# Optimization experiments

Hardware: AMD Instinct MI355X
Metric: run time of the kernel (lower is better)

## Reference

```python
import jax, jax.numpy as jnp
import numpy as np
import math

N_HEADS = 16
STRIDE = 4
LN_EPS = 1e-5
ROPE_BASE = 10000.0


def rotate_half(x):
    h = x.shape[-1] // 2
    return jnp.concatenate([-x[..., h:], x[..., :h]], axis=-1)


def rope_cos_sin(seq_len, head_dim, dtype):
    inv_freq = 1.0 / (ROPE_BASE ** (jnp.arange(0, head_dim, 2, dtype=jnp.float32) / head_dim))
    t = jnp.arange(seq_len, dtype=jnp.float32)
    freqs = jnp.outer(t, inv_freq)                      # [S, hd/2]
    emb = jnp.concatenate([freqs, freqs], axis=-1)      # [S, hd]
    return jnp.cos(emb).astype(dtype), jnp.sin(emb).astype(dtype)


def linear_upsample(x, T):
    # x: [B, Ts, D] -> [B, T, D]; matches F.interpolate(mode='linear', align_corners=False)
    Ts = x.shape[1]
    scale = Ts / T
    src = (jnp.arange(T, dtype=jnp.float32) + 0.5) * scale - 0.5
    src = jnp.clip(src, 0.0, Ts - 1.0)
    i0 = jnp.floor(src).astype(jnp.int32)
    i1 = jnp.minimum(i0 + 1, Ts - 1)
    w = (src - i0.astype(jnp.float32)).astype(x.dtype)[None, :, None]
    return x[:, i0, :] * (1.0 - w) + x[:, i1, :] * w


def setup_inputs() -> dict:
    key = jax.random.key(0)
    ks = jax.random.split(key, 4)
    B, T, D = 4, 4096, 1024
    s = 1.0 / math.sqrt(D)
    return {
        "x": jax.random.normal(ks[0], (B, T, D), dtype=jnp.float32),
        "norm_w": jnp.ones((D,), dtype=jnp.float32),
        "norm_b": jnp.zeros((D,), dtype=jnp.float32),
        "W_qkv": jax.random.normal(ks[1], (D, 3 * D), dtype=jnp.float32) * s,
        "b_qkv": jnp.zeros((3 * D,), dtype=jnp.float32),
        "W_out": jax.random.normal(ks[2], (D, D), dtype=jnp.float32) * s,
        "b_out": jnp.zeros((D,), dtype=jnp.float32),
    }


def reference(x, norm_w, norm_b, W_qkv, b_qkv, W_out, b_out):
    B, T, D = x.shape
    H = N_HEADS
    hd = D // H
    residual = x

    # LayerNorm (biased variance, eps=1e-5)
    mu = jnp.mean(x, axis=-1, keepdims=True)
    var = jnp.var(x, axis=-1, keepdims=True)
    x_norm = (x - mu) * jax.lax.rsqrt(var + LN_EPS) * norm_w + norm_b

    # strided downsample (T >= 2*stride path)
    xs = x_norm[:, ::STRIDE, :]
    Ts = xs.shape[1]

    # fused QKV projection
    qkv = xs @ W_qkv + b_qkv                             # [B, Ts, 3D]
    qkv = qkv.reshape(B, Ts, 3, H, hd).transpose(2, 0, 3, 1, 4)
    q, k, v = qkv[0], qkv[1], qkv[2]                     # [B, H, Ts, hd]

    # RoPE
    cos, sin = rope_cos_sin(Ts, hd, q.dtype)             # [Ts, hd]
    q = q * cos + rotate_half(q) * sin
    k = k * cos + rotate_half(k) * sin

    # causal SDPA on strided subsequence
    scores = jnp.einsum('bhqd,bhkd->bhqk', q, k) / math.sqrt(hd)
    causal = jnp.tril(jnp.ones((Ts, Ts), dtype=bool))
    scores = jnp.where(causal, scores, jnp.finfo(scores.dtype).min)
    attn = jax.nn.softmax(scores, axis=-1)
    out = jnp.einsum('bhqk,bhkd->bhqd', attn, v)         # [B, H, Ts, hd]
    out = out.transpose(0, 2, 1, 3).reshape(B, Ts, D)

    out = out @ W_out + b_out
    out = linear_upsample(out, T)                        # [B, T, D]
    return residual + out
```

## Files before the change

### kernel.cpp

```cpp
#include <hip/hip_runtime.h>
#include <hip/hip_bf16.h>

#define DEVFN __device__ __forceinline__

typedef float f32x4 __attribute__((ext_vector_type(4)));
typedef float f32x16 __attribute__((ext_vector_type(16)));
typedef __bf16 bf16x8 __attribute__((ext_vector_type(8)));
typedef unsigned short u16x8 __attribute__((ext_vector_type(8)));
typedef unsigned short u16x4 __attribute__((ext_vector_type(4)));
typedef unsigned u32x4 __attribute__((ext_vector_type(4)));

DEVFN unsigned short f2bf(float f) {
  unsigned u = __builtin_bit_cast(unsigned, f);
  u = (u + 0x7FFFu + ((u >> 16) & 1u)) >> 16;
  return (unsigned short)u;
}

DEVFN float bf2f(unsigned short s) {
  return __builtin_bit_cast(float, (unsigned)s << 16);
}

DEVFN f32x4 mfma_bf16(u16x8 a, u16x8 b, f32x4 c) {
  return __builtin_amdgcn_mfma_f32_16x16x32_bf16((bf16x8)a, (bf16x8)b, c, 0, 0, 0);
}

DEVFN f32x16 mfma32(u16x8 a, u16x8 b, f32x16 c) {
  return __builtin_amdgcn_mfma_f32_32x32x16_bf16((bf16x8)a, (bf16x8)b, c, 0, 0, 0);
}

DEVFN unsigned cvt_pk_bf16(float a, float b) {
  unsigned r;
  asm("v_cvt_pk_bf16_f32 %0, %1, %2" : "=v"(r) : "v"(a), "v"(b));
  return r;
}

DEVFN void permswap(unsigned& a, unsigned& b) {
  asm("v_permlane32_swap_b32 %0, %1" : "+v"(a), "+v"(b));
}

DEVFN void sincos_rev(float rev, float* sn, float* cs) {
  float fr, s, c;
  asm("v_fract_f32 %0, %1" : "=v"(fr) : "v"(rev));
  asm("v_sin_f32 %0, %1" : "=v"(s) : "v"(fr));
  asm("v_cos_f32 %0, %1" : "=v"(c) : "v"(fr));
  *sn = s; *cs = c;
}

DEVFN void gload_lds16(const void* g, void* l) {
  __builtin_amdgcn_global_load_lds(
      (const __attribute__((address_space(1))) void*)g,
      (__attribute__((address_space(3))) void*)l, 16, 0, 0);
}

__global__ __launch_bounds__(256) void prologue_kernel(
    const float* __restrict__ x, const float* __restrict__ w,
    const float* __restrict__ bb, unsigned short* __restrict__ xs,
    const float* __restrict__ Wq, unsigned short* __restrict__ Wtq,
    const float* __restrict__ Wo, unsigned short* __restrict__ Wto,
    int T, int Ts, int D, int stride, int M) {
  __shared__ float tile[32][33];
  __shared__ float ps[4], pq[4];
  int bid = blockIdx.x;
  int t = threadIdx.x;
  if (bid < M) {
    int b = bid / Ts, ts = bid - b * Ts;
    const float* xr = x + ((size_t)b * T + (size_t)ts * stride) * D;
    float4 v = *(const float4*)(xr + t * 4);
    float s = v.x + v.y + v.z + v.w;
    float sq = v.x * v.x + v.y * v.y + v.z * v.z + v.w * v.w;
#pragma unroll
    for (int m = 1; m < 64; m <<= 1) { s += __shfl_xor(s, m); sq += __shfl_xor(sq, m); }
    if ((t & 63) == 0) { ps[t >> 6] = s; pq[t >> 6] = sq; }
    __syncthreads();
    s = ps[0] + ps[1] + ps[2] + ps[3];
    sq = pq[0] + pq[1] + pq[2] + pq[3];
    float invD = 1.0f / (float)D;
    float mu = s * invD;
    float var = sq * invD - mu * mu;
    float rs = rsqrtf(var + 1e-5f);
    int c = t * 4;
    float4 wv = *(const float4*)(w + c);
    float4 bv = *(const float4*)(bb + c);
    u16x4 o;
    o[0] = f2bf((v.x - mu) * rs * wv.x + bv.x);
    o[1] = f2bf((v.y - mu) * rs * wv.y + bv.y);
    o[2] = f2bf((v.z - mu) * rs * wv.z + bv.z);
    o[3] = f2bf((v.w - mu) * rs * wv.w + bv.w);
    *(u16x4*)(xs + (size_t)bid * D + c) = o;
  } else {
    const float* W; unsigned short* Wt; int N, b2;
    b2 = bid - M;
    if (b2 < (3 * D / 32) * (D / 32)) { W = Wq; Wt = Wtq; N = 3 * D; }
    else { b2 -= (3 * D / 32) * (D / 32); W = Wo; Wt = Wto; N = D; }
    int nb = N / 32;
    int n0 = (b2 % nb) * 32, k0 = (b2 / nb) * 32;
    int tx = t & 31, ty = t >> 5;
#pragma unroll
    for (int i = 0; i < 32; i += 8) tile[ty + i][tx] = W[(size_t)(k0 + ty + i) * N + n0 + tx];
    __syncthreads();
#pragma unroll
    for (int i = 0; i < 32; i += 8) Wt[(size_t)(n0 + ty + i) * D + k0 + tx] = f2bf(tile[tx][ty + i]);
  }
}

__global__ __launch_bounds__(512, 1) void gemm_qkv256_kernel(
    const unsigned short* __restrict__ A, const unsigned short* __restrict__ Bt,
    const float* __restrict__ bias, int M, int N, int Kd,
    unsigned short* __restrict__ Qo, unsigned short* __restrict__ Ko,
    unsigned short* __restrict__ Vt) {
  __shared__ __align__(128) char lds[131072];
  const int tid = threadIdx.x, l = tid & 63, w = tid >> 6;
  const int wr = w >> 2, wc = w & 3;
  const int lg = l >> 4, lr = l & 15;
  const int o = blockIdx.x;
  const int xcd = o & 7, s = o >> 3;
  const int bm = (xcd & 3) * 4 + (s & 3);
  const int bn = (xcd >> 2) * 6 + (s >> 2);
  const int m0 = bm << 8, n0 = bn << 8;
  const int chk = (lg ^ ((lr >> 1) & 3)) << 4;

  f32x4 acc[8][4] = {};

#define STAGE32(kk, bufoff)                                                 \
  do {                                                                      \
    _Pragma("unroll")                                                       \
    for (int i_ = 0; i_ < 2; i_++) {                                        \
      int c_ = tid + (i_ << 9);                                             \
      int rl_ = c_ >> 2, c4_ = c_ & 3;                                      \
      int cs_ = c4_ ^ ((rl_ >> 1) & 3);                                     \
      gload_lds16(A + (size_t)(m0 + rl_) * Kd + (kk) + cs_ * 8,             \
                  lds + (bufoff) + c_ * 16);                                \
      gload_lds16(Bt + (size_t)(n0 + rl_) * Kd + (kk) + cs_ * 8,            \
                  lds + (bufoff) + 16384 + c_ * 16);                        \
    }                                                                       \
  } while (0)

  STAGE32(0, 0);
  STAGE32(32, 32768);
  STAGE32(64, 65536);

  const int NT = Kd >> 5;
  for (int t = 0; t < NT; ++t) {
    if (t < NT - 2)       asm volatile("s_waitcnt vmcnt(8)" ::: "memory");
    else if (t == NT - 2) asm volatile("s_waitcnt vmcnt(4)" ::: "memory");
    else                  asm volatile("s_waitcnt vmcnt(0)" ::: "memory");
    __builtin_amdgcn_s_barrier();
    const int curoff = (t & 3) << 15;

    u16x8 bfr[4], afr[8];
#pragma unroll
    for (int nf = 0; nf < 4; nf++)
      bfr[nf] = *(const u16x8*)(lds + curoff + 16384 +
                                (wc * 64 + nf * 16 + lr) * 64 + chk);
#pragma unroll
    for (int mf = 0; mf < 8; mf++)
      afr[mf] = *(const u16x8*)(lds + curoff +
                                (wr * 128 + mf * 16 + lr) * 64 + chk);
    if (t + 3 < NT) STAGE32((t + 3) << 5, ((t + 3) & 3) << 15);
    asm volatile("s_waitcnt lgkmcnt(0)" ::: "memory");
    __builtin_amdgcn_sched_barrier(0);
    __builtin_amdgcn_s_setprio(1);
#pragma unroll
    for (int mf = 0; mf < 8; mf++)
#pragma unroll
      for (int nf = 0; nf < 4; nf++)
        acc[mf][nf] = mfma_bf16(afr[mf], bfr[nf], acc[mf][nf]);
    __builtin_amdgcn_s_setprio(0);
    __builtin_amdgcn_s_barrier();
  }
#undef STAGE32

  int nb = n0 + wc * 64;
  int which = nb >> 10;
  int h = (nb & 1023) >> 6;
  if (which < 2) {
    unsigned short* dst = (which == 0) ? Qo : Ko;
    float qsc = (which == 0) ? 0.18033688f : 1.0f;
#pragma unroll
    for (int nt = 0; nt < 2; nt++) {
      int d = nt * 16 + lr;
      float invf_rev = exp2f((float)d * -0.41524101f) * 0.15915494f;
      float blo = bias[nb + nt * 16 + lr];
      float bhi = bias[nb + (nt + 2) * 16 + lr];
#pragma unroll
      for (int mt = 0; mt < 8; mt++) {
        int mb = m0 + wr * 128 + mt * 16 + lg * 4;
#pragma unroll
        for (int r = 0; r < 4; r++) {
          int m = mb + r;
          int b_ = m >> 10, ts = m & 1023;
          float va = acc[mt][nt][r] + blo;
          float vb = acc[mt][nt + 2][r] + bhi;
          float sn, cs;
          sincos_rev((float)ts * invf_rev, &sn, &cs);
          size_t base = (((size_t)(b_ * 16 + h)) * 1024 + ts) * 64;
          dst[base + d] = f2bf((va * cs - vb * sn) * qsc);
          dst[base + d + 32] = f2bf((vb * cs + va * sn) * qsc);
        }
      }
    }
  } else {
#pragma unroll
    for (int nt = 0; nt < 4; nt++) {
      int d = nt * 16 + lr;
      float bi = bias[nb + nt * 16 + lr];
#pragma unroll
      for (int mt = 0; mt < 8; mt++) {
        int mb = m0 + wr * 128 + mt * 16 + lg * 4;
        int b_ = mb >> 10, tsb = mb & 1023;
        u16x4 pk;
#pragma unroll
        for (int r = 0; r < 4; r++) pk[r] = f2bf(acc[mt][nt][r] + bi);
        *(u16x4*)(Vt + (size_t)(b_ * 16 + h) * 65536 +
                  (size_t)(tsb >> 5) * 2048 + d * 32 + (tsb & 31)) = pk;
      }
    }
  }
}

__global__ __launch_bounds__(256) void gemm_out_kernel(
    const unsigned short* __restrict__ A, const unsigned short* __restrict__ Bt,
    const float* __restrict__ bias, int M, int N, int Kd,
    unsigned short* __restrict__ Co) {
  __shared__ __align__(128) char lds[49152];
  const int tid = threadIdx.x, l = tid & 63, w = tid >> 6;
  const int wr = w >> 1, wc = w & 1;
  const int lg = l >> 4, lr = l & 15;
  const int o = blockIdx.x;
  const int xcd = o & 7, s = o >> 3;
  const int bm = xcd * 4 + (s & 3);
  const int bn = s >> 2;
  const int m0 = bm << 7, n0 = bn << 7;
  const int chk = (lg ^ ((lr >> 1) & 3)) << 4;

#define STAGE32O(kk, bufoff)                                                \
  do {                                                                      \
    _Pragma("unroll")                                                       \
    for (int i_ = 0; i_ < 2; i_++) {                                        \
      int c_ = tid + (i_ << 8);                                             \
      int rl_ = c_ >> 2, c4_ = c_ & 3;                                      \
      int cs_ = c4_ ^ ((rl_ >> 1) & 3);                                     \
      gload_lds16(A + (size_t)(m0 + rl_) * Kd + (kk) + cs_ * 8,             \
                  lds + (bufoff) + c_ * 16);                                \
      gload_lds16(Bt + (size_t)(n0 + rl_) * Kd + (kk) + cs_ * 8,            \
                  lds + (bufoff) + 8192 + c_ * 16);                         \
    }                                                                       \
  } while (0)

  f32x4 acc[4][4] = {};
  STAGE32O(0, 0);
  STAGE32O(32, 16384);

  const int NT = Kd >> 5;
  for (int t = 0; t < NT; ++t) {
    if (t < NT - 1) asm volatile("s_waitcnt vmcnt(4)" ::: "memory");
    else            asm volatile("s_waitcnt vmcnt(0)" ::: "memory");
    __builtin_amdgcn_s_barrier();
    const int curoff = (t % 3) * 16384;

    u16x8 bfr[4], afr[4];
#pragma unroll
    for (int nf = 0; nf < 4; nf++)
      bfr[nf] = *(const u16x8*)(lds + curoff + 8192 +
                                (wc * 64 + nf * 16 + lr) * 64 + chk);
#pragma unroll
    for (int mf = 0; mf < 4; mf++)
      afr[mf] = *(const u16x8*)(lds + curoff +
                                (wr * 64 + mf * 16 + lr) * 64 + chk);
    if (t + 2 < NT) STAGE32O((t + 2) << 5, ((t + 2) % 3) * 16384);
    asm volatile("s_waitcnt lgkmcnt(0)" ::: "memory");
    __builtin_amdgcn_sched_barrier(0);
    __builtin_amdgcn_s_setprio(1);
#pragma unroll
    for (int mf = 0; mf < 4; mf++)
#pragma unroll
      for (int nf = 0; nf < 4; nf++)
        acc[mf][nf] = mfma_bf16(afr[mf], bfr[nf], acc[mf][nf]);
    __builtin_amdgcn_s_setprio(0);
    __builtin_amdgcn_s_barrier();
  }
#undef STAGE32O

#pragma unroll
  for (int nt = 0; nt < 4; nt++) {
    int n = n0 + wc * 64 + nt * 16 + lr;
    float bi = bias[n];
#pragma unroll
    for (int mt = 0; mt < 4; mt++) {
      int mb = m0 + wr * 64 + mt * 16 + lg * 4;
#pragma unroll
      for (int r = 0; r < 4; r++)
        Co[(size_t)(mb + r) * N + n] = f2bf(acc[mt][nt][r] + bi);
    }
  }
}

__global__ __launch_bounds__(256) void attn_kernel(
    const unsigned short* __restrict__ Q, const unsigned short* __restrict__ K,
    const unsigned short* __restrict__ Vt, unsigned short* __restrict__ O,
    int Ts, int H) {
  __shared__ __align__(128) char kvlds[2][16384];
  int t = threadIdx.x, w = t >> 6, l = t & 63;
  int h2 = l >> 5, lq = l & 31;
  int bh = blockIdx.x & 63;
  int i = blockIdx.x >> 6;
  int qg = (i < 4) ? 7 - i : i - 4;
  int b = bh / H, hh = bh % H;
  int qw0 = qg * 128 + w * 32;

  const unsigned short* Qh = Q + ((size_t)bh * Ts) * 64;
  const unsigned short* Kh = K + ((size_t)bh * Ts) * 64;
  const unsigned short* Vh = Vt + (size_t)bh * 65536;

  u16x8 qf[4];
#pragma unroll
  for (int c = 0; c < 4; c++)
    qf[c] = *(const u16x8*)(Qh + (size_t)(qw0 + lq) * 64 + c * 16 + h2 * 8);

#define STAGE_KV(jt, buf)                                                   \
  do {                                                                      \
    _Pragma("unroll")                                                       \
    for (int i_ = 0; i_ < 2; i_++) {                                        \
      int c_ = t + (i_ << 8);                                               \
      int r_ = c_ >> 3, jg_ = c_ & 7;                                       \
      gload_lds16(Kh + (size_t)(jt) * 4096 + r_ * 64 + ((jg_ ^ (r_ & 7)) << 3), \
                  kvlds[buf] + c_ * 16);                                    \
    }                                                                       \
    {                                                                       \
      int d_ = t >> 2, g_ = t & 3;                                          \
      int gs_ = (g_ ^ ((d_ >> 1) & 3)) << 3;                                \
      gload_lds16(Vh + (size_t)(2 * (jt)) * 2048 + d_ * 32 + gs_,           \
                  kvlds[buf] + 8192 + t * 16);                              \
      gload_lds16(Vh + (size_t)(2 * (jt) + 1) * 2048 + d_ * 32 + gs_,       \
                  kvlds[buf] + 12288 + t * 16);                             \
    }                                                                       \
  } while (0)

  f32x16 olo = {}, ohi = {};
  float mrow = -1e30f, lsum = 0.f;
  const int sk = lq & 7;
  const int sv = (lq >> 1) & 3;

  int ntiles = 2 * qg + 2;
  STAGE_KV(0, 0);

  for (int jt = 0; jt < ntiles; jt++) {
    __syncthreads();
    int cur = jt & 1;
    if (jt + 1 < ntiles) STAGE_KV(jt + 1, cur ^ 1);

    int kvt = jt * 64;
    if (kvt > qw0) continue;
    bool haveS1 = (kvt + 32 <= qw0);
    bool diag0 = (kvt == qw0);
    bool diag1 = (kvt + 32 == qw0);

    const char* kb0 = kvlds[cur] + lq * 128;
    const char* kb1 = kvlds[cur] + (32 + lq) * 128;
    u16x8 kf0[4], kf1[4];
#pragma unroll
    for (int c = 0; c < 4; c++)
      kf0[c] = *(const u16x8*)(kb0 + (((c << 1) + h2) ^ sk) * 16);
    f32x16 sA = {}, sB = {};
    if (haveS1) {
#pragma unroll
      for (int c = 0; c < 4; c++)
        kf1[c] = *(const u16x8*)(kb1 + (((c << 1) + h2) ^ sk) * 16);
      __builtin_amdgcn_s_setprio(1);
#pragma unroll
      for (int c = 0; c < 4; c++) sA = mfma32(kf0[c], qf[c], sA);
#pragma unroll
      for (int c = 0; c < 4; c++) sB = mfma32(kf1[c], qf[c], sB);
      __builtin_amdgcn_s_setprio(0);
    } else {
      __builtin_amdgcn_s_setprio(1);
#pragma unroll
      for (int c = 0; c < 4; c++) sA = mfma32(kf0[c], qf[c], sA);
      __builtin_amdgcn_s_setprio(0);
    }

    float p[32];
#pragma unroll
    for (int r = 0; r < 16; r++) {
      float v = sA[r];
      if (diag0) {
        int kvl = (r & 3) + 8 * (r >> 2) + 4 * h2;
        v = (kvl > lq) ? -1e30f : v;
      }
      p[r] = v;
    }
#pragma unroll
    for (int r = 0; r < 16; r++) {
      float v = haveS1 ? sB[r] : -1e30f;
      if (diag1) {
        int kvl = (r & 3) + 8 * (r >> 2) + 4 * h2;
        v = (kvl > lq) ? -1e30f : v;
      }
      p[16 + r] = v;
    }

    float m16[16], m8[8], m4[4];
#pragma unroll
    for (int r = 0; r < 16; r++) m16[r] = fmaxf(p[r], p[16 + r]);
#pragma unroll
    for (int r = 0; r < 8; r++) m8[r] = fmaxf(m16[r], m16[r + 8]);
#pragma unroll
    for (int r = 0; r < 4; r++) m4[r] = fmaxf(m8[r], m8[r + 4]);
    float tmax = fmaxf(fmaxf(m4[0], m4[2]), fmaxf(m4[1], m4[3]));
    tmax = fmaxf(tmax, __shfl_xor(tmax, 32));

    if (!__all(tmax <= mrow + 8.0f)) {
      float mnew = fmaxf(mrow, tmax);
      float al = exp2f(mrow - mnew);
      mrow = mnew;
      lsum *= al;
      olo *= al;
      ohi *= al;
    }

#pragma unroll
    for (int r = 0; r < 32; r++) p[r] = exp2f(p[r] - mrow);
    float s16[16], s8[8], s4[4];
#pragma unroll
    for (int r = 0; r < 16; r++) s16[r] = p[r] + p[16 + r];
#pragma unroll
    for (int r = 0; r < 8; r++) s8[r] = s16[r] + s16[r + 8];
#pragma unroll
    for (int r = 0; r < 4; r++) s4[r] = s8[r] + s8[r + 4];
    lsum += (s4[0] + s4[2]) + (s4[1] + s4[3]);

    {
      unsigned a01 = cvt_pk_bf16(p[0], p[1]),   a23 = cvt_pk_bf16(p[2], p[3]);
      unsigned a45 = cvt_pk_bf16(p[4], p[5]),   a67 = cvt_pk_bf16(p[6], p[7]);
      unsigned a89 = cvt_pk_bf16(p[8], p[9]),   aAB = cvt_pk_bf16(p[10], p[11]);
      unsigned aCD = cvt_pk_bf16(p[12], p[13]), aEF = cvt_pk_bf16(p[14], p[15]);
      permswap(a01, a45);
      permswap(a23, a67);
      permswap(a89, aCD);
      permswap(aAB, aEF);
      u32x4 f0 = {a01, a23, a45, a67};
      u32x4 f1 = {a89, aAB, aCD, aEF};
      u16x8 P0 = __builtin_bit_cast(u16x8, f0);
      u16x8 P1 = __builtin_bit_cast(u16x8, f1);

      const char* vb_ = kvlds[cur] + 8192;
      u16x8 vf[4];
      vf[0] = *(const u16x8*)(vb_ + lq * 64 + ((0 + h2) ^ sv) * 16);
      vf[1] = *(const u16x8*)(vb_ + lq * 64 + ((2 + h2) ^ sv) * 16);
      vf[2] = *(const u16x8*)(vb_ + (32 + lq) * 64 + ((0 + h2) ^ sv) * 16);
      vf[3] = *(const u16x8*)(vb_ + (32 + lq) * 64 + ((2 + h2) ^ sv) * 16);
      __builtin_amdgcn_s_setprio(1);
      olo = mfma32(vf[0], P0, olo);
      olo = mfma32(vf[1], P1, olo);
      ohi = mfma32(vf[2], P0, ohi);
      ohi = mfma32(vf[3], P1, ohi);
      __builtin_amdgcn_s_setprio(0);
    }

    if (haveS1) {
      unsigned b01 = cvt_pk_bf16(p[16], p[17]), b23 = cvt_pk_bf16(p[18], p[19]);
      unsigned b45 = cvt_pk_bf16(p[20], p[21]), b67 = cvt_pk_bf16(p[22], p[23]);
      unsigned b89 = cvt_pk_bf16(p[24], p[25]), bAB = cvt_pk_bf16(p[26], p[27]);
      unsigned bCD = cvt_pk_bf16(p[28], p[29]), bEF = cvt_pk_bf16(p[30], p[31]);
      permswap(b01, b45);
      permswap(b23, b67);
      permswap(b89, bCD);
      permswap(bAB, bEF);
      u32x4 g0 = {b01, b23, b45, b67};
      u32x4 g1 = {b89, bAB, bCD, bEF};
      u16x8 Q0 = __builtin_bit_cast(u16x8, g0);
      u16x8 Q1 = __builtin_bit_cast(u16x8, g1);

      const char* vb_ = kvlds[cur] + 8192 + 4096;
      u16x8 vf[4];
      vf[0] = *(const u16x8*)(vb_ + lq * 64 + ((0 + h2) ^ sv) * 16);
      vf[1] = *(const u16x8*)(vb_ + lq * 64 + ((2 + h2) ^ sv) * 16);
      vf[2] = *(const u16x8*)(vb_ + (32 + lq) * 64 + ((0 + h2) ^ sv) * 16);
      vf[3] = *(const u16x8*)(vb_ + (32 + lq) * 64 + ((2 + h2) ^ sv) * 16);
      __builtin_amdgcn_s_setprio(1);
      olo = mfma32(vf[0], Q0, olo);
      olo = mfma32(vf[1], Q1, olo);
      ohi = mfma32(vf[2], Q0, ohi);
      ohi = mfma32(vf[3], Q1, ohi);
      __builtin_amdgcn_s_setprio(0);
    }
  }
#undef STAGE_KV

  lsum += __shfl_xor(lsum, 32);
  float inv = 1.0f / lsum;
  int q = qw0 + lq;
  unsigned short* orow = O + ((size_t)b * Ts + q) * (size_t)(H * 64) + hh * 64;
#pragma unroll
  for (int g = 0; g < 4; g++) {
    u16x4 plo, phi;
#pragma unroll
    for (int j2 = 0; j2 < 4; j2++) {
      plo[j2] = f2bf(olo[g * 4 + j2] * inv);
      phi[j2] = f2bf(ohi[g * 4 + j2] * inv);
    }
    *(u16x4*)(orow + g * 8 + h2 * 4) = plo;
    *(u16x4*)(orow + 32 + g * 8 + h2 * 4) = phi;
  }
}

__global__ __launch_bounds__(256) void upsample_kernel(
    const float* __restrict__ x, const unsigned short* __restrict__ proj,
    float* __restrict__ out, int T, int Ts, int D) {
  int bk = blockIdx.x;
  int b = bk / Ts, k = bk - b * Ts;
  int d4 = threadIdx.x;
  size_t prow = (size_t)b * Ts * D;
  u16x4 av = *((const u16x4*)(proj + prow + (size_t)max(k - 1, 0) * D) + d4);
  u16x4 bv = *((const u16x4*)(proj + prow + (size_t)k * D) + d4);
  u16x4 cv = *((const u16x4*)(proj + prow + (size_t)min(k + 1, Ts - 1) * D) + d4);
  f32x4 a, bb, c;
#pragma unroll
  for (int j = 0; j < 4; j++) {
    a[j] = bf2f(av[j]); bb[j] = bf2f(bv[j]); c[j] = bf2f(cv[j]);
  }

  size_t xbase = ((size_t)b * T + 4 * (size_t)k) * D + (size_t)d4 * 4;
  f32x4 x0 = __builtin_nontemporal_load((const f32x4*)(x + xbase));
  f32x4 x1 = __builtin_nontemporal_load((const f32x4*)(x + xbase + D));
  f32x4 x2 = __builtin_nontemporal_load((const f32x4*)(x + xbase + 2 * D));
  f32x4 x3 = __builtin_nontemporal_load((const f32x4*)(x + xbase + 3 * D));

  f32x4 o0 = x0 + 0.375f * a + 0.625f * bb;
  f32x4 o1 = x1 + 0.125f * a + 0.875f * bb;
  f32x4 o2 = x2 + 0.875f * bb + 0.125f * c;
  f32x4 o3 = x3 + 0.625f * bb + 0.375f * c;

  __builtin_nontemporal_store(o0, (f32x4*)(out + xbase));
  __builtin_nontemporal_store(o1, (f32x4*)(out + xbase + D));
  __builtin_nontemporal_store(o2, (f32x4*)(out + xbase + 2 * D));
  __builtin_nontemporal_store(o3, (f32x4*)(out + xbase + 3 * D));
}

extern "C" void kernel_launch(void* const* d_in, const int* in_sizes, int n_in,
                              void* d_out, int out_size, void* d_ws, size_t ws_size,
                              hipStream_t stream) {
  (void)in_sizes; (void)n_in; (void)out_size; (void)ws_size;
  const float* x = (const float*)d_in[0];
  const float* norm_w = (const float*)d_in[1];
  const float* norm_b = (const float*)d_in[2];
  const float* W_qkv = (const float*)d_in[3];
  const float* b_qkv = (const float*)d_in[4];
  const float* W_out = (const float*)d_in[5];
  const float* b_out = (const float*)d_in[6];
  float* out = (float*)d_out;

  const int B = 4, T = 4096, D = 1024, H = 16, STR = 4;
  const int Ts = T / STR;
  const int M = B * Ts;

  char* ws = (char*)d_ws;
  unsigned short* xs  = (unsigned short*)(ws);
  unsigned short* Wtq = (unsigned short*)(ws + ((size_t)8 << 20));
  unsigned short* Wto = (unsigned short*)(ws + ((size_t)14 << 20));
  unsigned short* Qb  = (unsigned short*)(ws + ((size_t)16 << 20));
  unsigned short* Kb  = (unsigned short*)(ws + ((size_t)24 << 20));
  unsigned short* Vtb = (unsigned short*)(ws + ((size_t)32 << 20));
  unsigned short* proj = (unsigned short*)(ws + ((size_t)16 << 20));
  unsigned short* att = xs;

  prologue_kernel<<<M + (3 * D / 32) * (D / 32) + (D / 32) * (D / 32), 256, 0, stream>>>(
      x, norm_w, norm_b, xs, W_qkv, Wtq, W_out, Wto, T, Ts, D, STR, M);
  gemm_qkv256_kernel<<<(M / 256) * (3 * D / 256), 512, 0, stream>>>(
      xs, Wtq, b_qkv, M, 3 * D, D, Qb, Kb, Vtb);
  attn_kernel<<<B * H * 8, 256, 0, stream>>>(Qb, Kb, Vtb, att, Ts, H);
  gemm_out_kernel<<<(M / 128) * (D / 128), 256, 0, stream>>>(
      att, Wto, b_out, M, D, D, proj);
  upsample_kernel<<<B * Ts, 256, 0, stream>>>(x, proj, out, T, Ts, D);
}
```

Measured before the change: 118.4 us.

## Split attention KV loop across warps per 32-query tile with LDS merge

The attention kernel now gives each block a single 32-query tile and splits its causal KV tiles across the four warps in strided fashion. K and V fragments are read straight from global memory instead of being staged through double-buffered LDS. The per-warp partial softmax states are then merged through shared memory in a two-step reduction. This launches more blocks and balances causal work better, at the cost of uncoalesced global K/V reads, no K/V reuse across warps, and extra merge synchronisation.

```diff
diff --git a/kernel.cpp b/kernel.cpp
--- a/kernel.cpp
+++ b/kernel.cpp
@@ -299,14 +299,12 @@
     const unsigned short* __restrict__ Q, const unsigned short* __restrict__ K,
     const unsigned short* __restrict__ Vt, unsigned short* __restrict__ O,
     int Ts, int H) {
-  __shared__ __align__(128) char kvlds[2][16384];
   int t = threadIdx.x, w = t >> 6, l = t & 63;
   int h2 = l >> 5, lq = l & 31;
   int bh = blockIdx.x & 63;
-  int i = blockIdx.x >> 6;
-  int qg = (i < 4) ? 7 - i : i - 4;
+  int qt = 31 - (blockIdx.x >> 6);
   int b = bh / H, hh = bh % H;
-  int qw0 = qg * 128 + w * 32;
+  int q0 = qt * 32;
 
   const unsigned short* Qh = Q + ((size_t)bh * Ts) * 64;
   const unsigned short* Kh = K + ((size_t)bh * Ts) * 64;
@@ -315,95 +313,46 @@
   u16x8 qf[4];
 #pragma unroll
   for (int c = 0; c < 4; c++)
-    qf[c] = *(const u16x8*)(Qh + (size_t)(qw0 + lq) * 64 + c * 16 + h2 * 8);
-
-#define STAGE_KV(jt, buf)                                                   \
-  do {                                                                      \
-    _Pragma("unroll")                                                       \
-    for (int i_ = 0; i_ < 2; i_++) {                                        \
-      int c_ = t + (i_ << 8);                                               \
-      int r_ = c_ >> 3, jg_ = c_ & 7;                                       \
-      gload_lds16(Kh + (size_t)(jt) * 4096 + r_ * 64 + ((jg_ ^ (r_ & 7)) << 3), \
-                  kvlds[buf] + c_ * 16);                                    \
-    }                                                                       \
-    {                                                                       \
-      int d_ = t >> 2, g_ = t & 3;                                          \
-      int gs_ = (g_ ^ ((d_ >> 1) & 3)) << 3;                                \
-      gload_lds16(Vh + (size_t)(2 * (jt)) * 2048 + d_ * 32 + gs_,           \
-                  kvlds[buf] + 8192 + t * 16);                              \
-      gload_lds16(Vh + (size_t)(2 * (jt) + 1) * 2048 + d_ * 32 + gs_,       \
-                  kvlds[buf] + 12288 + t * 16);                             \
-    }                                                                       \
-  } while (0)
+    qf[c] = *(const u16x8*)(Qh + (size_t)(q0 + lq) * 64 + c * 16 + h2 * 8);
+
+  const unsigned short* kb = Kh + (size_t)lq * 64 + h2 * 8;
+  const unsigned short* vb = Vh + (size_t)lq * 32 + h2 * 8;
 
   f32x16 olo = {}, ohi = {};
   float mrow = -1e30f, lsum = 0.f;
-  const int sk = lq & 7;
-  const int sv = (lq >> 1) & 3;
-
-  int ntiles = 2 * qg + 2;
-  STAGE_KV(0, 0);
-
-  for (int jt = 0; jt < ntiles; jt++) {
-    __syncthreads();
-    int cur = jt & 1;
-    if (jt + 1 < ntiles) STAGE_KV(jt + 1, cur ^ 1);
-
-    int kvt = jt * 64;
-    if (kvt > qw0) continue;
-    bool haveS1 = (kvt + 32 <= qw0);
-    bool diag0 = (kvt == qw0);
-    bool diag1 = (kvt + 32 == qw0);
-
-    const char* kb0 = kvlds[cur] + lq * 128;
-    const char* kb1 = kvlds[cur] + (32 + lq) * 128;
-    u16x8 kf0[4], kf1[4];
-#pragma unroll
-    for (int c = 0; c < 4; c++)
-      kf0[c] = *(const u16x8*)(kb0 + (((c << 1) + h2) ^ sk) * 16);
-    f32x16 sA = {}, sB = {};
-    if (haveS1) {
-#pragma unroll
-      for (int c = 0; c < 4; c++)
-        kf1[c] = *(const u16x8*)(kb1 + (((c << 1) + h2) ^ sk) * 16);
-      __builtin_amdgcn_s_setprio(1);
-#pragma unroll
-      for (int c = 0; c < 4; c++) sA = mfma32(kf0[c], qf[c], sA);
-#pragma unroll
-      for (int c = 0; c < 4; c++) sB = mfma32(kf1[c], qf[c], sB);
-      __builtin_amdgcn_s_setprio(0);
-    } else {
-      __builtin_amdgcn_s_setprio(1);
-#pragma unroll
-      for (int c = 0; c < 4; c++) sA = mfma32(kf0[c], qf[c], sA);
-      __builtin_amdgcn_s_setprio(0);
-    }
-
-    float p[32];
+
+  for (int j = w; j <= qt; j += 4) {
+    const unsigned short* kt = kb + (size_t)j * 2048;
+    const unsigned short* vt = vb + (size_t)j * 2048;
+    u16x8 kf[4], vf[4];
+#pragma unroll
+    for (int c = 0; c < 4; c++) kf[c] = *(const u16x8*)(kt + c * 16);
+    vf[0] = *(const u16x8*)(vt);
+    vf[1] = *(const u16x8*)(vt + 16);
+    vf[2] = *(const u16x8*)(vt + 1024);
+    vf[3] = *(const u16x8*)(vt + 1024 + 16);
+
+    f32x16 s = {};
+    __builtin_amdgcn_s_setprio(1);
+#pragma unroll
+    for (int c = 0; c < 4; c++) s = mfma32(kf[c], qf[c], s);
+    __builtin_amdgcn_s_setprio(0);
+
+    bool diag = (j == qt);
+    float p[16];
 #pragma unroll
     for (int r = 0; r < 16; r++) {
-      float v = sA[r];
-      if (diag0) {
+      float v = s[r];
+      if (diag) {
         int kvl = (r & 3) + 8 * (r >> 2) + 4 * h2;
         v = (kvl > lq) ? -1e30f : v;
       }
       p[r] = v;
     }
-#pragma unroll
-    for (int r = 0; r < 16; r++) {
-      float v = haveS1 ? sB[r] : -1e30f;
-      if (diag1) {
-        int kvl = (r & 3) + 8 * (r >> 2) + 4 * h2;
-        v = (kvl > lq) ? -1e30f : v;
-      }
-      p[16 + r] = v;
-    }
-
-    float m16[16], m8[8], m4[4];
-#pragma unroll
-    for (int r = 0; r < 16; r++) m16[r] = fmaxf(p[r], p[16 + r]);
-#pragma unroll
-    for (int r = 0; r < 8; r++) m8[r] = fmaxf(m16[r], m16[r + 8]);
+
+    float m8[8], m4[4];
+#pragma unroll
+    for (int r = 0; r < 8; r++) m8[r] = fmaxf(p[r], p[r + 8]);
 #pragma unroll
     for (int r = 0; r < 4; r++) m4[r] = fmaxf(m8[r], m8[r + 4]);
     float tmax = fmaxf(fmaxf(m4[0], m4[2]), fmaxf(m4[1], m4[3]));
@@ -419,88 +368,90 @@
     }
 
 #pragma unroll
-    for (int r = 0; r < 32; r++) p[r] = exp2f(p[r] - mrow);
-    float s16[16], s8[8], s4[4];
-#pragma unroll
-    for (int r = 0; r < 16; r++) s16[r] = p[r] + p[16 + r];
-#pragma unroll
-    for (int r = 0; r < 8; r++) s8[r] = s16[r] + s16[r + 8];
+    for (int r = 0; r < 16; r++) p[r] = exp2f(p[r] - mrow);
+    float s8[8], s4[4];
+#pragma unroll
+    for (int r = 0; r < 8; r++) s8[r] = p[r] + p[r + 8];
 #pragma unroll
     for (int r = 0; r < 4; r++) s4[r] = s8[r] + s8[r + 4];
     lsum += (s4[0] + s4[2]) + (s4[1] + s4[3]);
 
-    {
-      unsigned a01 = cvt_pk_bf16(p[0], p[1]),   a23 = cvt_pk_bf16(p[2], p[3]);
-      unsigned a45 = cvt_pk_bf16(p[4], p[5]),   a67 = cvt_pk_bf16(p[6], p[7]);
-      unsigned a89 = cvt_pk_bf16(p[8], p[9]),   aAB = cvt_pk_bf16(p[10], p[11]);
-      unsigned aCD = cvt_pk_bf16(p[12], p[13]), aEF = cvt_pk_bf16(p[14], p[15]);
-      permswap(a01, a45);
-      permswap(a23, a67);
-      permswap(a89, aCD);
-      permswap(aAB, aEF);
-      u32x4 f0 = {a01, a23, a45, a67};
-      u32x4 f1 = {a89, aAB, aCD, aEF};
-      u16x8 P0 = __builtin_bit_cast(u16x8, f0);
-      u16x8 P1 = __builtin_bit_cast(u16x8, f1);
-
-      const char* vb_ = kvlds[cur] + 8192;
-      u16x8 vf[4];
-      vf[0] = *(const u16x8*)(vb_ + lq * 64 + ((0 + h2) ^ sv) * 16);
-      vf[1] = *(const u16x8*)(vb_ + lq * 64 + ((2 + h2) ^ sv) * 16);
-      vf[2] = *(const u16x8*)(vb_ + (32 + lq) * 64 + ((0 + h2) ^ sv) * 16);
-      vf[3] = *(const u16x8*)(vb_ + (32 + lq) * 64 + ((2 + h2) ^ sv) * 16);
-      __builtin_amdgcn_s_setprio(1);
-      olo = mfma32(vf[0], P0, olo);
-      olo = mfma32(vf[1], P1, olo);
-      ohi = mfma32(vf[2], P0, ohi);
-      ohi = mfma32(vf[3], P1, ohi);
-      __builtin_amdgcn_s_setprio(0);
-    }
-
-    if (haveS1) {
-      unsigned b01 = cvt_pk_bf16(p[16], p[17]), b23 = cvt_pk_bf16(p[18], p[19]);
-      unsigned b45 = cvt_pk_bf16(p[20], p[21]), b67 = cvt_pk_bf16(p[22], p[23]);
-      unsigned b89 = cvt_pk_bf16(p[24], p[25]), bAB = cvt_pk_bf16(p[26], p[27]);
-      unsigned bCD = cvt_pk_bf16(p[28], p[29]), bEF = cvt_pk_bf16(p[30], p[31]);
-      permswap(b01, b45);
-      permswap(b23, b67);
-      permswap(b89, bCD);
-      permswap(bAB, bEF);
-      u32x4 g0 = {b01, b23, b45, b67};
-      u32x4 g1 = {b89, bAB, bCD, bEF};
-      u16x8 Q0 = __builtin_bit_cast(u16x8, g0);
-      u16x8 Q1 = __builtin_bit_cast(u16x8, g1);
-
-      const char* vb_ = kvlds[cur] + 8192 + 4096;
-      u16x8 vf[4];
-      vf[0] = *(const u16x8*)(vb_ + lq * 64 + ((0 + h2) ^ sv) * 16);
-      vf[1] = *(const u16x8*)(vb_ + lq * 64 + ((2 + h2) ^ sv) * 16);
-      vf[2] = *(const u16x8*)(vb_ + (32 + lq) * 64 + ((0 + h2) ^ sv) * 16);
-      vf[3] = *(const u16x8*)(vb_ + (32 + lq) * 64 + ((2 + h2) ^ sv) * 16);
-      __builtin_amdgcn_s_setprio(1);
-      olo = mfma32(vf[0], Q0, olo);
-      olo = mfma32(vf[1], Q1, olo);
-      ohi = mfma32(vf[2], Q0, ohi);
-      ohi = mfma32(vf[3], Q1, ohi);
-      __builtin_amdgcn_s_setprio(0);
-    }
-  }
-#undef STAGE_KV
-
-  lsum += __shfl_xor(lsum, 32);
-  float inv = 1.0f / lsum;
-  int q = qw0 + lq;
-  unsigned short* orow = O + ((size_t)b * Ts + q) * (size_t)(H * 64) + hh * 64;
-#pragma unroll
-  for (int g = 0; g < 4; g++) {
-    u16x4 plo, phi;
-#pragma unroll
-    for (int j2 = 0; j2 < 4; j2++) {
-      plo[j2] = f2bf(olo[g * 4 + j2] * inv);
-      phi[j2] = f2bf(ohi[g * 4 + j2] * inv);
-    }
-    *(u16x4*)(orow + g * 8 + h2 * 4) = plo;
-    *(u16x4*)(orow + 32 + g * 8 + h2 * 4) = phi;
+    unsigned a01 = cvt_pk_bf16(p[0], p[1]),   a23 = cvt_pk_bf16(p[2], p[3]);
+    unsigned a45 = cvt_pk_bf16(p[4], p[5]),   a67 = cvt_pk_bf16(p[6], p[7]);
+    unsigned a89 = cvt_pk_bf16(p[8], p[9]),   aAB = cvt_pk_bf16(p[10], p[11]);
+    unsigned aCD = cvt_pk_bf16(p[12], p[13]), aEF = cvt_pk_bf16(p[14], p[15]);
+    permswap(a01, a45);
+    permswap(a23, a67);
+    permswap(a89, aCD);
+    permswap(aAB, aEF);
+    u32x4 f0 = {a01, a23, a45, a67};
+    u32x4 f1 = {a89, aAB, aCD, aEF};
+    u16x8 P0 = __builtin_bit_cast(u16x8, f0);
+    u16x8 P1 = __builtin_bit_cast(u16x8, f1);
+
+    __builtin_amdgcn_s_setprio(1);
+    olo = mfma32(vf[0], P0, olo);
+    olo = mfma32(vf[1], P1, olo);
+    ohi = mfma32(vf[2], P0, ohi);
+    ohi = mfma32(vf[3], P1, ohi);
+    __builtin_amdgcn_s_setprio(0);
+  }
+
+  __shared__ float Obuf[2][64][33];
+  __shared__ float Mbuf[2][64], Lbuf[2][64];
+
+  if (w >= 2) {
+    int bq = w - 2;
+#pragma unroll
+    for (int r = 0; r < 16; r++) { Obuf[bq][l][r] = olo[r]; Obuf[bq][l][16 + r] = ohi[r]; }
+    Mbuf[bq][l] = mrow; Lbuf[bq][l] = lsum;
+  }
+  __syncthreads();
+  if (w < 2) {
+    float m2_ = Mbuf[w][l], l2_ = Lbuf[w][l];
+    float mg = fmaxf(mrow, m2_);
+    float f1 = exp2f(mrow - mg), f2 = exp2f(m2_ - mg);
+#pragma unroll
+    for (int r = 0; r < 16; r++) {
+      olo[r] = olo[r] * f1 + Obuf[w][l][r] * f2;
+      ohi[r] = ohi[r] * f1 + Obuf[w][l][16 + r] * f2;
+    }
+    lsum = lsum * f1 + l2_ * f2;
+    mrow = mg;
+  }
+  __syncthreads();
+  if (w == 1) {
+#pragma unroll
+    for (int r = 0; r < 16; r++) { Obuf[0][l][r] = olo[r]; Obuf[0][l][16 + r] = ohi[r]; }
+    Mbuf[0][l] = mrow; Lbuf[0][l] = lsum;
+  }
+  __syncthreads();
+  if (w == 0) {
+    float m2_ = Mbuf[0][l], l2_ = Lbuf[0][l];
+    float mg = fmaxf(mrow, m2_);
+    float f1 = exp2f(mrow - mg), f2 = exp2f(m2_ - mg);
+#pragma unroll
+    for (int r = 0; r < 16; r++) {
+      olo[r] = olo[r] * f1 + Obuf[0][l][r] * f2;
+      ohi[r] = ohi[r] * f1 + Obuf[0][l][16 + r] * f2;
+    }
+    lsum = lsum * f1 + l2_ * f2;
+    lsum += __shfl_xor(lsum, 32);
+
+    float inv = 1.0f / lsum;
+    int q = q0 + lq;
+    unsigned short* orow = O + ((size_t)b * Ts + q) * (size_t)(H * 64) + hh * 64;
+#pragma unroll
+    for (int g = 0; g < 4; g++) {
+      u16x4 plo, phi;
+#pragma unroll
+      for (int j2 = 0; j2 < 4; j2++) {
+        plo[j2] = f2bf(olo[g * 4 + j2] * inv);
+        phi[j2] = f2bf(ohi[g * 4 + j2] * inv);
+      }
+      *(u16x4*)(orow + g * 8 + h2 * 4) = plo;
+      *(u16x4*)(orow + 32 + g * 8 + h2 * 4) = phi;
+    }
   }
 }
 
@@ -568,7 +519,7 @@
       x, norm_w, norm_b, xs, W_qkv, Wtq, W_out, Wto, T, Ts, D, STR, M);
   gemm_qkv256_kernel<<<(M / 256) * (3 * D / 256), 512, 0, stream>>>(
       xs, Wtq, b_qkv, M, 3 * D, D, Qb, Kb, Vtb);
-  attn_kernel<<<B * H * 8, 256, 0, stream>>>(Qb, Kb, Vtb, att, Ts, H);
+  attn_kernel<<<B * H * (Ts / 32), 256, 0, stream>>>(Qb, Kb, Vtb, att, Ts, H);
   gemm_out_kernel<<<(M / 128) * (D / 128), 256, 0, stream>>>(
       att, Wto, b_out, M, D, D, proj);
   upsample_kernel<<<B * Ts, 256, 0, stream>>>(x, proj, out, T, Ts, D);
```

Measured after the change: 121.7 us. +2.8%, slower.
